# Performance work log

Hardware: AMD Instinct MI355X
Metric: run time of the kernel (lower is better)

## Reference

```python
import jax, jax.numpy as jnp
import numpy as np

N_NODES = 100000


def setup_inputs() -> dict:
    key = jax.random.key(0)
    k1, k2, k3, k4, k5, k6 = jax.random.split(key, 6)
    N, E, F_IN, F_OUT = N_NODES, 1600000, 128, 128
    stdv = 1.0 / np.sqrt(F_OUT)
    return {
        "input_features": jax.random.normal(k1, (N, F_IN), dtype=jnp.float32),
        "edge_row": jnp.sort(jax.random.randint(k2, (E,), 0, N, dtype=jnp.int32)),
        "edge_col": jax.random.randint(k3, (E,), 0, N, dtype=jnp.int32),
        "edge_val": jax.random.uniform(k4, (E,), dtype=jnp.float32),
        "weight": jax.random.uniform(k5, (F_IN, F_OUT), minval=-stdv, maxval=stdv, dtype=jnp.float32),
        "bias": jax.random.uniform(k6, (F_OUT,), minval=-stdv, maxval=stdv, dtype=jnp.float32),
    }


def reference(input_features, edge_row, edge_col, edge_val, weight, bias):
    # support = X @ W   [N, F_out]  (dense GEMM)
    support = jnp.matmul(input_features, weight)
    # output = spmm(adj, support): COO adjacency, segment-sum over destination rows
    msgs = edge_val[:, None] * support[edge_col]          # [E, F_out] gather
    output = jax.ops.segment_sum(msgs, edge_row, num_segments=N_NODES)
    return output + bias
```

## Files before the change

### kernel.cpp

```cpp
#include <hip/hip_runtime.h>

typedef unsigned int uint;
typedef unsigned short ushort;
typedef unsigned char uchar;
typedef unsigned long long ull;
typedef __attribute__((ext_vector_type(4))) float f32x4;
typedef __attribute__((ext_vector_type(4))) uint u32x4;
typedef __attribute__((ext_vector_type(2))) uint u32x2;

#define NNODES 100000
#define NPAD   100032
#define NEDGES 1600000
#define FD 128
#define BM 64

__device__ __forceinline__ uint cvt_pk_bf16(float lo, float hi) {
    uint r;
    asm("v_cvt_pk_bf16_f32 %0, %1, %2" : "=v"(r) : "v"(lo), "v"(hi));
    return r;
}
__device__ __forceinline__ int swz(int row, int k) {
    return (row * 256 + k * 2) ^ ((row & 7) << 4);
}

__global__ __launch_bounds__(256) void prep(const float* __restrict__ W,
                                            ushort* __restrict__ Wt,
                                            const int* __restrict__ rows,
                                            int* __restrict__ ptr) {
    const int bid = blockIdx.x;
    if (bid < 16) {
        const int sid = bid * 256 + threadIdx.x;
        const int n = sid & 127, k0 = (sid >> 7) * 4;
        const float w0 = W[(k0 + 0) * FD + n];
        const float w1 = W[(k0 + 1) * FD + n];
        const float w2 = W[(k0 + 2) * FD + n];
        const float w3 = W[(k0 + 3) * FD + n];
        u32x2 p;
        p.x = cvt_pk_bf16(w0, w1);
        p.y = cvt_pk_bf16(w2, w3);
        *(u32x2*)((char*)Wt + swz(n, k0)) = p;
    } else {
        const int r = (bid - 16) * 256 + threadIdx.x;
        if (r > NNODES) return;
        int lo = 0, hi = NEDGES;
        while (lo < hi) {
            const int mid = (lo + hi) >> 1;
            const bool lt = rows[mid] < r;
            lo = lt ? mid + 1 : lo;
            hi = lt ? hi : mid;
        }
        ptr[r] = lo;
    }
}

__global__ __launch_bounds__(256) void gemm_mfma_q8(const float* __restrict__ X,
                                                    const ushort* __restrict__ Wt,
                                                    uchar* __restrict__ S8,
                                                    float* __restrict__ scale) {
    __shared__ ushort As[BM * FD];
    __shared__ ushort Bs[FD * FD];
    const int tid = threadIdx.x;
    const int row0 = blockIdx.x * BM;

    #pragma unroll
    for (int it = 0; it < 8; ++it) {
        const int idx = tid + it * 256;
        const int r = idx >> 5, k0 = (idx & 31) * 4;
        const int grow = min(row0 + r, NNODES - 1);
        const float4 g = *(const float4*)&X[grow * FD + k0];
        u32x2 p;
        p.x = cvt_pk_bf16(g.x, g.y);
        p.y = cvt_pk_bf16(g.z, g.w);
        *(u32x2*)((char*)As + swz(r, k0)) = p;
    }
    #pragma unroll
    for (int it = 0; it < 8; ++it) {
        const int b = (tid + it * 256) * 16;
        *(u32x4*)((char*)Bs + b) = *(const u32x4*)((const char*)Wt + b);
    }
    __syncthreads();

    const int lane = tid & 63, wv = tid >> 6;
    const int l15 = lane & 15, kg = lane >> 4;
    const int arow = wv * 16 + l15;

    f32x4 acc[8];
    #pragma unroll
    for (int i = 0; i < 8; ++i) acc[i] = (f32x4)0.f;

    #pragma unroll
    for (int ks = 0; ks < 4; ++ks) {
        const int k0 = ks * 32 + kg * 8;
        const u32x4 a = *(const u32x4*)((const char*)As + swz(arow, k0));
        #pragma unroll
        for (int nf = 0; nf < 8; ++nf) {
            const u32x4 b = *(const u32x4*)((const char*)Bs + swz(nf * 16 + l15, k0));
            asm volatile("v_mfma_f32_16x16x32_bf16 %0, %1, %2, %0"
                         : "+v"(acc[nf]) : "v"(a), "v"(b));
        }
    }
    asm volatile("s_nop 7\ns_nop 7\ns_nop 7");

    __syncthreads();
    uchar* As8 = (uchar*)As;

    #pragma unroll
    for (int r = 0; r < 4; ++r) {
        float m = 0.f;
        #pragma unroll
        for (int nf = 0; nf < 8; ++nf) m = fmaxf(m, fabsf(acc[nf][r]));
        m = fmaxf(m, __shfl_xor(m, 1));
        m = fmaxf(m, __shfl_xor(m, 2));
        m = fmaxf(m, __shfl_xor(m, 4));
        m = fmaxf(m, __shfl_xor(m, 8));
        m = fmaxf(m, 1e-20f);
        const int lrow = wv * 16 + kg * 4 + r;
        if (l15 == 0) scale[row0 + lrow] = m * (1.f / 127.f);
        const float inv = 127.f / m;
        #pragma unroll
        for (int nf = 0; nf < 8; ++nf) {
            const int q = (int)rintf(acc[nf][r] * inv) + 128;
            As8[lrow * FD + nf * 16 + l15] = (uchar)q;
        }
    }
    __syncthreads();
    #pragma unroll
    for (int it = 0; it < 2; ++it) {
        const int o = (tid + it * 256) * 16;
        *(u32x4*)(S8 + (size_t)row0 * FD + o) = *(const u32x4*)(As8 + o);
    }
}

__global__ __launch_bounds__(256) void build_vs(const int* __restrict__ ecol,
                                                const float* __restrict__ eval_,
                                                const float* __restrict__ scale,
                                                float* __restrict__ VS) {
    const int i = blockIdx.x * 256 + threadIdx.x;
    if (i < NEDGES) VS[i] = eval_[i] * scale[ecol[i]];
}

__global__ __launch_bounds__(256, 8) void spmm_row(const int* __restrict__ rptr,
                                                   const int* __restrict__ ecol,
                                                   const float* __restrict__ VS,
                                                   const uchar* __restrict__ S8,
                                                   const float* __restrict__ bias,
                                                   float* __restrict__ out) {
    const int row = (blockIdx.x * 256 + threadIdx.x) >> 6;
    const int lane = threadIdx.x & 63;
    const float2 b2 = *(const float2*)&bias[lane * 2];

    const int E0 = __builtin_amdgcn_readfirstlane(rptr[row]);
    const int E1 = __builtin_amdgcn_readfirstlane(rptr[row + 1]);

    const int ml = lane & 15;
    const uint* mb = (lane & 16) ? (const uint*)VS : (const uint*)ecol;
    const uint voff = (uint)lane << 1;

    float a00 = 0.f, a01 = 0.f, a10 = 0.f, a11 = 0.f;
    float sv0 = 0.f, sv1 = 0.f;

    const int nc = (E1 - E0 + 15) >> 4;
    if (nc > 0) {

#define LOADMETA(m, c) { \
        const int i_ = min(E0 + (c) * 16 + ml, E1 - 1); \
        m = mb[i_]; }

#define STAGE(G, V, m, c) { \
        _Pragma("unroll") for (int j = 0; j < 16; ++j) { \
            const uint cj = (uint)__builtin_amdgcn_readlane((int)(m), j); \
            G[j] = (uint)*(const ushort*)(S8 + ((size_t)cj << 7) + voff); \
            const uint uv = (uint)__builtin_amdgcn_readlane((int)(m), 16 + j); \
            const uint uz = (E0 + (c) * 16 + j < E1) ? uv : 0u;   \
            V[j] = __uint_as_float(uz); } }

#define PROC(G, V) { \
        _Pragma("unroll") for (int j = 0; j < 16; ++j) { \
            const float lo_ = (float)(G[j] & 0xffu); \
            const float hi_ = (float)((G[j] >> 8) & 0xffu); \
            if (j & 1) { a10 = fmaf(V[j], lo_, a10); \
                         a11 = fmaf(V[j], hi_, a11); sv1 += V[j]; } \
            else       { a00 = fmaf(V[j], lo_, a00); \
                         a01 = fmaf(V[j], hi_, a01); sv0 += V[j]; } } }

        uint mA, mB = 0;
        uint gA[16], gB[16];
        float vA[16], vB[16];

        LOADMETA(mA, 0);
        STAGE(gA, vA, mA, 0);
        if (nc > 1) LOADMETA(mB, 1);

        int c = 0;
        while (true) {
            if (c + 1 < nc) STAGE(gB, vB, mB, c + 1);
            if (c + 2 < nc) LOADMETA(mA, c + 2);
            PROC(gA, vA);
            if (++c >= nc) break;
            if (c + 1 < nc) STAGE(gA, vA, mA, c + 1);
            if (c + 2 < nc) LOADMETA(mB, c + 2);
            PROC(gB, vB);
            if (++c >= nc) break;
        }
#undef PROC
#undef STAGE
#undef LOADMETA
    }

    const float sv = sv0 + sv1;
    float2 o;
    o.x = fmaf(-128.f, sv, a00 + a10) + b2.x;
    o.y = fmaf(-128.f, sv, a01 + a11) + b2.y;
    *(float2*)&out[(size_t)row * FD + voff] = o;
}

extern "C" void kernel_launch(void* const* d_in, const int* in_sizes, int n_in,
                              void* d_out, int out_size, void* d_ws, size_t ws_size,
                              hipStream_t stream) {
    const float* X    = (const float*)d_in[0];
    const int*   erow = (const int*)d_in[1];
    const int*   ecol = (const int*)d_in[2];
    const float* eval_= (const float*)d_in[3];
    const float* W    = (const float*)d_in[4];
    const float* bias = (const float*)d_in[5];
    float* out = (float*)d_out;

    uchar* S8    = (uchar*)d_ws;
    float* scale = (float*)((char*)d_ws + 13u * 1024 * 1024);
    int*   rpt   = (int*)((char*)d_ws + 14u * 1024 * 1024);
    float* VS    = (float*)((char*)d_ws + 15u * 1024 * 1024);
    ushort* Wt   = (ushort*)((char*)d_ws + 22u * 1024 * 1024);

    prep<<<16 + (NNODES + 256) / 256, 256, 0, stream>>>(W, Wt, erow, rpt);
    gemm_mfma_q8<<<NPAD / BM, 256, 0, stream>>>(X, Wt, S8, scale);
    build_vs<<<(NEDGES + 255) / 256, 256, 0, stream>>>(ecol, eval_, scale, VS);
    spmm_row<<<NNODES / 4, 256, 0, stream>>>(rpt, ecol, VS, S8, bias, out);
}
```

Before: 86.96 us.

## Split row edges across lane pairs with packed col/value metadata and 4-byte gathers

Packs each edge's column index and scaled value into one 8-byte record, so every lane loads its own metadata directly instead of broadcasting it with readlane. The SpMM now has each wave handle 2 edges at a time: each half-wave gathers 4 int8 features per edge (a 4-byte load) for alternating edges, and the two partial sums are combined with a shuffle at the end. The aim is to cut readlane/scalar overhead and the number of gather instructions per edge. In exchange the metadata buffer doubles in size, and only half the lanes store the final output.

```diff
diff --git a/kernel.cpp b/kernel.cpp
--- a/kernel.cpp
+++ b/kernel.cpp
@@ -3,7 +3,6 @@
 typedef unsigned int uint;
 typedef unsigned short ushort;
 typedef unsigned char uchar;
-typedef unsigned long long ull;
 typedef __attribute__((ext_vector_type(4))) float f32x4;
 typedef __attribute__((ext_vector_type(4))) uint u32x4;
 typedef __attribute__((ext_vector_type(2))) uint u32x2;
@@ -131,87 +130,141 @@
     }
 }
 
-__global__ __launch_bounds__(256) void build_vs(const int* __restrict__ ecol,
-                                                const float* __restrict__ eval_,
-                                                const float* __restrict__ scale,
-                                                float* __restrict__ VS) {
+__global__ __launch_bounds__(256) void build_meta(const int* __restrict__ ecol,
+                                                  const float* __restrict__ eval_,
+                                                  const float* __restrict__ scale,
+                                                  u32x2* __restrict__ Meta) {
     const int i = blockIdx.x * 256 + threadIdx.x;
-    if (i < NEDGES) VS[i] = eval_[i] * scale[ecol[i]];
-}
-
-__global__ __launch_bounds__(256, 8) void spmm_row(const int* __restrict__ rptr,
-                                                   const int* __restrict__ ecol,
-                                                   const float* __restrict__ VS,
-                                                   const uchar* __restrict__ S8,
-                                                   const float* __restrict__ bias,
-                                                   float* __restrict__ out) {
+    if (i < NEDGES) {
+        const int c = ecol[i];
+        u32x2 m;
+        m.x = (uint)c;
+        m.y = __float_as_uint(eval_[i] * scale[c]);
+        Meta[i] = m;
+    }
+}
+
+__global__ __launch_bounds__(256, 8) void spmm_pair(const int* __restrict__ rptr,
+                                                    const u32x2* __restrict__ Meta,
+                                                    const uchar* __restrict__ S8,
+                                                    const float* __restrict__ bias,
+                                                    float* __restrict__ out) {
     const int row = (blockIdx.x * 256 + threadIdx.x) >> 6;
     const int lane = threadIdx.x & 63;
-    const float2 b2 = *(const float2*)&bias[lane * 2];
+    const int h = lane & 1;
+    const int q = lane >> 1;
+    const uint voff = (uint)q << 2;
 
     const int E0 = __builtin_amdgcn_readfirstlane(rptr[row]);
     const int E1 = __builtin_amdgcn_readfirstlane(rptr[row + 1]);
-
-    const int ml = lane & 15;
-    const uint* mb = (lane & 16) ? (const uint*)VS : (const uint*)ecol;
-    const uint voff = (uint)lane << 1;
-
-    float a00 = 0.f, a01 = 0.f, a10 = 0.f, a11 = 0.f;
-    float sv0 = 0.f, sv1 = 0.f;
-
-    const int nc = (E1 - E0 + 15) >> 4;
+    const float4 b4 = *(const float4*)&bias[q * 4];
+
+    float a0 = 0.f, a1 = 0.f, a2 = 0.f, a3 = 0.f, sv = 0.f;
+
+    const int nc = (E1 - E0 + 7) >> 3;
     if (nc > 0) {
 
-#define LOADMETA(m, c) { \
-        const int i_ = min(E0 + (c) * 16 + ml, E1 - 1); \
-        m = mb[i_]; }
-
-#define STAGE(G, V, m, c) { \
-        _Pragma("unroll") for (int j = 0; j < 16; ++j) { \
-            const uint cj = (uint)__builtin_amdgcn_readlane((int)(m), j); \
-            G[j] = (uint)*(const ushort*)(S8 + ((size_t)cj << 7) + voff); \
-            const uint uv = (uint)__builtin_amdgcn_readlane((int)(m), 16 + j); \
-            const uint uz = (E0 + (c) * 16 + j < E1) ? uv : 0u;   \
-            V[j] = __uint_as_float(uz); } }
-
-#define PROC(G, V) { \
-        _Pragma("unroll") for (int j = 0; j < 16; ++j) { \
-            const float lo_ = (float)(G[j] & 0xffu); \
-            const float hi_ = (float)((G[j] >> 8) & 0xffu); \
-            if (j & 1) { a10 = fmaf(V[j], lo_, a10); \
-                         a11 = fmaf(V[j], hi_, a11); sv1 += V[j]; } \
-            else       { a00 = fmaf(V[j], lo_, a00); \
-                         a01 = fmaf(V[j], hi_, a01); sv0 += V[j]; } } }
-
-        uint mA, mB = 0;
-        uint gA[16], gB[16];
-        float vA[16], vB[16];
+#define LOADMETA(M_, c) { \
+        _Pragma("unroll") for (int pp = 0; pp < 4; ++pp) { \
+            const int e_ = min(E0 + (c) * 8 + 2 * pp + h, E1 - 1); \
+            M_[pp] = Meta[e_]; } }
+
+#define GATHER(G_, M_) { \
+        _Pragma("unroll") for (int pp = 0; pp < 4; ++pp) { \
+            G_[pp] = *(const uint*)(S8 + ((size_t)M_[pp].x << 7) + voff); } }
+
+#define PROC1(g_, vv_) { \
+        a0 = fmaf(vv_, (float)( (g_)        & 0xffu), a0); \
+        a1 = fmaf(vv_, (float)(((g_) >>  8) & 0xffu), a1); \
+        a2 = fmaf(vv_, (float)(((g_) >> 16) & 0xffu), a2); \
+        a3 = fmaf(vv_, (float)( (g_) >> 24        ),  a3); \
+        sv += vv_; }
+
+#define PROC(G_, M_) { \
+        _Pragma("unroll") for (int pp = 0; pp < 4; ++pp) { \
+            const float vv = __uint_as_float(M_[pp].y); \
+            PROC1(G_[pp], vv) } }
+
+#define PROC_TAIL(G_, M_, c) { \
+        _Pragma("unroll") for (int pp = 0; pp < 4; ++pp) { \
+            const int e_ = E0 + (c) * 8 + 2 * pp + h; \
+            float vv = __uint_as_float(M_[pp].y); \
+            vv = (e_ < E1) ? vv : 0.f; \
+            PROC1(G_[pp], vv) } }
+
+#define BODY(MC, MN, GC, GN, c) { \
+        if ((c) + 1 < nc) GATHER(GN, MN); \
+        if ((c) + 2 < nc) LOADMETA(MC, (c) + 2); \
+        if ((c) == nc - 1) { PROC_TAIL(GC, MC##save, c) } \
+        else { PROC(GC, MC##save) } }
+
+        u32x2 mA[4], mB[4];
+        uint gA[4], gB[4];
 
         LOADMETA(mA, 0);
-        STAGE(gA, vA, mA, 0);
+        GATHER(gA, mA);
         if (nc > 1) LOADMETA(mB, 1);
 
         int c = 0;
         while (true) {
-            if (c + 1 < nc) STAGE(gB, vB, mB, c + 1);
+            float vvA[4];
+            #pragma unroll
+            for (int pp = 0; pp < 4; ++pp) vvA[pp] = __uint_as_float(mA[pp].y);
+            if (c + 1 < nc) GATHER(gB, mB);
             if (c + 2 < nc) LOADMETA(mA, c + 2);
-            PROC(gA, vA);
+            if (c == nc - 1) {
+                #pragma unroll
+                for (int pp = 0; pp < 4; ++pp) {
+                    const int e_ = E0 + c * 8 + 2 * pp + h;
+                    const float vv = (e_ < E1) ? vvA[pp] : 0.f;
+                    PROC1(gA[pp], vv)
+                }
+            } else {
+                #pragma unroll
+                for (int pp = 0; pp < 4; ++pp) PROC1(gA[pp], vvA[pp])
+            }
             if (++c >= nc) break;
-            if (c + 1 < nc) STAGE(gA, vA, mA, c + 1);
+
+            float vvB[4];
+            #pragma unroll
+            for (int pp = 0; pp < 4; ++pp) vvB[pp] = __uint_as_float(mB[pp].y);
+            if (c + 1 < nc) GATHER(gA, mA);
             if (c + 2 < nc) LOADMETA(mB, c + 2);
-            PROC(gB, vB);
+            if (c == nc - 1) {
+                #pragma unroll
+                for (int pp = 0; pp < 4; ++pp) {
+                    const int e_ = E0 + c * 8 + 2 * pp + h;
+                    const float vv = (e_ < E1) ? vvB[pp] : 0.f;
+                    PROC1(gB[pp], vv)
+                }
+            } else {
+                #pragma unroll
+                for (int pp = 0; pp < 4; ++pp) PROC1(gB[pp], vvB[pp])
+            }
             if (++c >= nc) break;
         }
+#undef BODY
+#undef PROC_TAIL
 #undef PROC
-#undef STAGE
+#undef PROC1
+#undef GATHER
 #undef LOADMETA
     }
 
-    const float sv = sv0 + sv1;
-    float2 o;
-    o.x = fmaf(-128.f, sv, a00 + a10) + b2.x;
-    o.y = fmaf(-128.f, sv, a01 + a11) + b2.y;
-    *(float2*)&out[(size_t)row * FD + voff] = o;
+    a0 += __shfl_xor(a0, 1);
+    a1 += __shfl_xor(a1, 1);
+    a2 += __shfl_xor(a2, 1);
+    a3 += __shfl_xor(a3, 1);
+    sv += __shfl_xor(sv, 1);
+
+    if (h == 0) {
+        float4 o;
+        o.x = fmaf(-128.f, sv, a0) + b4.x;
+        o.y = fmaf(-128.f, sv, a1) + b4.y;
+        o.z = fmaf(-128.f, sv, a2) + b4.z;
+        o.w = fmaf(-128.f, sv, a3) + b4.w;
+        *(float4*)&out[(size_t)row * FD + (q << 2)] = o;
+    }
 }
 
 extern "C" void kernel_launch(void* const* d_in, const int* in_sizes, int n_in,
@@ -228,11 +281,11 @@
     uchar* S8    = (uchar*)d_ws;
     float* scale = (float*)((char*)d_ws + 13u * 1024 * 1024);
     int*   rpt   = (int*)((char*)d_ws + 14u * 1024 * 1024);
-    float* VS    = (float*)((char*)d_ws + 15u * 1024 * 1024);
-    ushort* Wt   = (ushort*)((char*)d_ws + 22u * 1024 * 1024);
+    u32x2* Meta  = (u32x2*)((char*)d_ws + 15u * 1024 * 1024);
+    ushort* Wt   = (ushort*)((char*)d_ws + 28u * 1024 * 1024);
 
     prep<<<16 + (NNODES + 256) / 256, 256, 0, stream>>>(W, Wt, erow, rpt);
     gemm_mfma_q8<<<NPAD / BM, 256, 0, stream>>>(X, Wt, S8, scale);
-    build_vs<<<(NEDGES + 255) / 256, 256, 0, stream>>>(ecol, eval_, scale, VS);
-    spmm_row<<<NNODES / 4, 256, 0, stream>>>(rpt, ecol, VS, S8, bias, out);
-}
+    build_meta<<<(NEDGES + 255) / 256, 256, 0, stream>>>(ecol, eval_, scale, Meta);
+    spmm_pair<<<NNODES / 4, 256, 0, stream>>>(rpt, Meta, S8, bias, out);
+}
```

Measured after the change: 176.4 us. 2.03x slower.

## Process eight rows per wavefront as one merged edge stream in SpMM

Applied to the files above, without the earlier changes.

The SpMM kernel now gives each wavefront a contiguous range of eight destination rows and walks their edges as a single stream. It detects row changes from erow loaded alongside ecol and VS in the metadata lane groups, and flushes the accumulator whenever the row changes. Empty rows are written with bias afterwards. The aim is to remove per-row pipeline startup and the idle lanes on short rows, which leave latency exposed since rows average about 16 edges. A triple-buffered metadata rotation and nontemporal loads and stores are added. The cost is a per-edge branch on row change, and four times fewer wavefronts in flight, which may reduce latency hiding.

```diff
diff --git a/kernel.cpp b/kernel.cpp
--- a/kernel.cpp
+++ b/kernel.cpp
@@ -5,6 +5,7 @@
 typedef unsigned char uchar;
 typedef unsigned long long ull;
 typedef __attribute__((ext_vector_type(4))) float f32x4;
+typedef __attribute__((ext_vector_type(2))) float f32x2;
 typedef __attribute__((ext_vector_type(4))) uint u32x4;
 typedef __attribute__((ext_vector_type(2))) uint u32x2;
 
@@ -13,6 +14,7 @@
 #define NEDGES 1600000
 #define FD 128
 #define BM 64
+#define RPW 8
 
 __device__ __forceinline__ uint cvt_pk_bf16(float lo, float hi) {
     uint r;
@@ -139,79 +141,103 @@
     if (i < NEDGES) VS[i] = eval_[i] * scale[ecol[i]];
 }
 
-__global__ __launch_bounds__(256, 8) void spmm_row(const int* __restrict__ rptr,
-                                                   const int* __restrict__ ecol,
-                                                   const float* __restrict__ VS,
-                                                   const uchar* __restrict__ S8,
-                                                   const float* __restrict__ bias,
-                                                   float* __restrict__ out) {
-    const int row = (blockIdx.x * 256 + threadIdx.x) >> 6;
+__global__ __launch_bounds__(256, 8) void spmm16(const int* __restrict__ rptr,
+                                                 const int* __restrict__ erow,
+                                                 const int* __restrict__ ecol,
+                                                 const float* __restrict__ VS,
+                                                 const uchar* __restrict__ S8,
+                                                 const float* __restrict__ bias,
+                                                 float* __restrict__ out) {
+    const int wv = (blockIdx.x * 256 + threadIdx.x) >> 6;
     const int lane = threadIdx.x & 63;
-    const float2 b2 = *(const float2*)&bias[lane * 2];
-
-    const int E0 = __builtin_amdgcn_readfirstlane(rptr[row]);
-    const int E1 = __builtin_amdgcn_readfirstlane(rptr[row + 1]);
+    const int r0 = wv * RPW;
+    const f32x2 b2 = *(const f32x2*)&bias[lane * 2];
+    const uint voff = (uint)lane << 1;
+
+    const int E0 = __builtin_amdgcn_readfirstlane(rptr[r0]);
+    const int E1 = __builtin_amdgcn_readfirstlane(rptr[r0 + RPW]);
 
     const int ml = lane & 15;
-    const uint* mb = (lane & 16) ? (const uint*)VS : (const uint*)ecol;
-    const uint voff = (uint)lane << 1;
-
-    float a00 = 0.f, a01 = 0.f, a10 = 0.f, a11 = 0.f;
-    float sv0 = 0.f, sv1 = 0.f;
-
-    const int nc = (E1 - E0 + 15) >> 4;
-    if (nc > 0) {
-
-#define LOADMETA(m, c) { \
-        const int i_ = min(E0 + (c) * 16 + ml, E1 - 1); \
-        m = mb[i_]; }
-
-#define STAGE(G, V, m, c) { \
+    const uint* mb = (lane < 16) ? (const uint*)ecol
+                   : (lane < 32) ? (const uint*)VS
+                                 : (const uint*)erow;
+
+    float a0 = 0.f, a1 = 0.f, sv = 0.f;
+
+    if (E0 < E1) {
+        const int nb = (E1 - E0 + 15) >> 4;
+        int rcur = __builtin_amdgcn_readfirstlane(erow[E0]);
+
+#define LOADMETA(M_, b_) { \
+        const int i_ = min(E0 + (b_) * 16 + ml, NEDGES - 1); \
+        M_ = __builtin_nontemporal_load(&mb[i_]); }
+
+#define GATHER(G_, M_) { \
         _Pragma("unroll") for (int j = 0; j < 16; ++j) { \
-            const uint cj = (uint)__builtin_amdgcn_readlane((int)(m), j); \
-            G[j] = (uint)*(const ushort*)(S8 + ((size_t)cj << 7) + voff); \
-            const uint uv = (uint)__builtin_amdgcn_readlane((int)(m), 16 + j); \
-            const uint uz = (E0 + (c) * 16 + j < E1) ? uv : 0u;   \
-            V[j] = __uint_as_float(uz); } }
-
-#define PROC(G, V) { \
+            const uint c_ = (uint)__builtin_amdgcn_readlane((int)(M_), j); \
+            G_[j] = (uint)*(const ushort*)(S8 + ((size_t)c_ << 7) + voff); } }
+
+#define FLUSH() { f32x2 o_; \
+        o_.x = fmaf(-128.f, sv, a0) + b2.x; \
+        o_.y = fmaf(-128.f, sv, a1) + b2.y; \
+        __builtin_nontemporal_store(o_, (f32x2*)&out[(size_t)rcur * FD + voff]); \
+        a0 = 0.f; a1 = 0.f; sv = 0.f; }
+
+#define EDGE(gj, M_, j) { \
+        const int rj = __builtin_amdgcn_readlane((int)(M_), 32 + j); \
+        const float vj = __int_as_float(__builtin_amdgcn_readlane((int)(M_), 16 + j)); \
+        if (rj != rcur) { FLUSH(); rcur = rj; } \
+        a0 = fmaf(vj, (float)(gj & 0xffu), a0); \
+        a1 = fmaf(vj, (float)(gj >> 8), a1); \
+        sv += vj; }
+
+#define PROC(G_, M_) { \
+        _Pragma("unroll") for (int j = 0; j < 16; ++j) { EDGE(G_[j], M_, j) } }
+
+#define PROC_LAST(G_, M_, b_) { \
         _Pragma("unroll") for (int j = 0; j < 16; ++j) { \
-            const float lo_ = (float)(G[j] & 0xffu); \
-            const float hi_ = (float)((G[j] >> 8) & 0xffu); \
-            if (j & 1) { a10 = fmaf(V[j], lo_, a10); \
-                         a11 = fmaf(V[j], hi_, a11); sv1 += V[j]; } \
-            else       { a00 = fmaf(V[j], lo_, a00); \
-                         a01 = fmaf(V[j], hi_, a01); sv0 += V[j]; } } }
-
-        uint mA, mB = 0;
+            if (E0 + (b_) * 16 + j < E1) { EDGE(G_[j], M_, j) } } }
+
+#define STEP(GC, GN, MC, MN, ML, b_) { \
+        if ((b_) + 1 < nb) GATHER(GN, MN); \
+        if ((b_) + 2 < nb) LOADMETA(ML, (b_) + 2); \
+        if ((b_) == nb - 1) { PROC_LAST(GC, MC, b_) } else { PROC(GC, MC) } }
+
+        uint mA, mB = 0, mC = 0;
         uint gA[16], gB[16];
-        float vA[16], vB[16];
 
         LOADMETA(mA, 0);
-        STAGE(gA, vA, mA, 0);
-        if (nc > 1) LOADMETA(mB, 1);
-
-        int c = 0;
+        LOADMETA(mB, 1);
+        GATHER(gA, mA);
+
+        int b = 0;
         while (true) {
-            if (c + 1 < nc) STAGE(gB, vB, mB, c + 1);
-            if (c + 2 < nc) LOADMETA(mA, c + 2);
-            PROC(gA, vA);
-            if (++c >= nc) break;
-            if (c + 1 < nc) STAGE(gA, vA, mA, c + 1);
-            if (c + 2 < nc) LOADMETA(mB, c + 2);
-            PROC(gB, vB);
-            if (++c >= nc) break;
-        }
+            STEP(gA, gB, mA, mB, mC, b); if (++b >= nb) break;
+            STEP(gB, gA, mB, mC, mA, b); if (++b >= nb) break;
+            STEP(gA, gB, mC, mA, mB, b); if (++b >= nb) break;
+            STEP(gB, gA, mA, mB, mC, b); if (++b >= nb) break;
+            STEP(gA, gB, mB, mC, mA, b); if (++b >= nb) break;
+            STEP(gB, gA, mC, mA, mB, b); if (++b >= nb) break;
+        }
+        FLUSH();
+
+#undef STEP
+#undef PROC_LAST
 #undef PROC
-#undef STAGE
+#undef EDGE
+#undef FLUSH
+#undef GATHER
 #undef LOADMETA
     }
 
-    const float sv = sv0 + sv1;
-    float2 o;
-    o.x = fmaf(-128.f, sv, a00 + a10) + b2.x;
-    o.y = fmaf(-128.f, sv, a01 + a11) + b2.y;
-    *(float2*)&out[(size_t)row * FD + voff] = o;
+    const int rl = r0 + ((lane < RPW) ? lane : RPW - 1);
+    const bool em = (lane < RPW) && (rptr[rl] == rptr[rl + 1]);
+    ull mask = __ballot(em);
+    while (mask) {
+        const int i = __ffsll(mask) - 1;
+        mask &= mask - 1;
+        __builtin_nontemporal_store(b2, (f32x2*)&out[(size_t)(r0 + i) * FD + voff]);
+    }
 }
 
 extern "C" void kernel_launch(void* const* d_in, const int* in_sizes, int n_in,
@@ -234,5 +260,5 @@
     prep<<<16 + (NNODES + 256) / 256, 256, 0, stream>>>(W, Wt, erow, rpt);
     gemm_mfma_q8<<<NPAD / BM, 256, 0, stream>>>(X, Wt, S8, scale);
     build_vs<<<(NEDGES + 255) / 256, 256, 0, stream>>>(ecol, eval_, scale, VS);
-    spmm_row<<<NNODES / 4, 256, 0, stream>>>(rpt, ecol, VS, S8, bias, out);
-}
+    spmm16<<<NNODES / RPW / 4, 256, 0, stream>>>(rpt, erow, ecol, VS, S8, bias, out);
+}
```

Measured after the change: 97.08 us. 11.6% more time.
